# Performance work log

Measured on AMD Instinct MI355X. Metric: run time of the kernel, lower is better.

Reference implementation:

```python
import jax, jax.numpy as jnp
import numpy as np

N_HEAD = 8
N_VIEWS = 26
C = 256
H = W = 32
B_SCENE = 2


def _get_default_angles():
    # Reconstructed: bottom pole, top pole, then 3 rings of 8 azimuths at elev 45/0/-45.
    angs = [(0.0, -90.0), (0.0, 90.0)]
    for phi in (45.0, 0.0, -45.0):
        for k in range(8):
            angs.append((45.0 * k, phi))
    return np.array(angs)


def _angle_select():
    a = _get_default_angles()
    d = np.abs(a.reshape(26, 1, 2) - a.reshape(1, 26, 2))
    d = np.sum(np.minimum(d, 360 - d), axis=2)
    ab = d == 45
    ab[0, -8::2] = True
    ab[-8::2, 0] = True
    ab[1, 2:10:2] = True
    ab[2:10:2, 1] = True
    return [np.argwhere(ab[i]).reshape(-1) for i in range(26)]


def _mha_index(i):
    return i if i < 2 else (i - 2) // 8 + 2


def _mha(q, kv, Wqkv, bqkv, Wo, bo):
    # torch nn.MultiheadAttention, batch_first: packed in_proj, scale = 1/sqrt(head_dim)
    c = q.shape[-1]
    D = c // N_HEAD
    Wq, Wk, Wv = Wqkv[:c], Wqkv[c:2 * c], Wqkv[2 * c:]
    bq, bk, bv = bqkv[:c], bqkv[c:2 * c], bqkv[2 * c:]
    qp = q @ Wq.T + bq
    kp = kv @ Wk.T + bk
    vp = kv @ Wv.T + bv
    B, S, _ = qp.shape
    K = kp.shape[1]
    qh = qp.reshape(B, S, N_HEAD, D).transpose(0, 2, 1, 3)
    kh = kp.reshape(B, K, N_HEAD, D).transpose(0, 2, 1, 3)
    vh = vp.reshape(B, K, N_HEAD, D).transpose(0, 2, 1, 3)
    scores = jnp.einsum('bhqd,bhkd->bhqk', qh, kh) / jnp.sqrt(jnp.asarray(D, qh.dtype))
    att = jax.nn.softmax(scores, axis=-1)
    o = jnp.einsum('bhqk,bhkd->bhqd', att, vh).transpose(0, 2, 1, 3).reshape(B, S, c)
    return o @ Wo.T + bo


def setup_inputs() -> dict:
    key = jax.random.key(0)
    k1, k2, k3 = jax.random.split(key, 3)
    scale = 1.0 / np.sqrt(C)
    return {
        'x': jax.random.normal(k1, (B_SCENE * N_VIEWS, C, H, W), dtype=jnp.float32),
        'w_qkv': jax.random.normal(k2, (5, 3 * C, C), dtype=jnp.float32) * scale,
        'b_qkv': jnp.zeros((5, 3 * C), dtype=jnp.float32),
        'w_out': jax.random.normal(k3, (5, C, C), dtype=jnp.float32) * scale,
        'b_out': jnp.zeros((5, C), dtype=jnp.float32),
    }


def reference(x, w_qkv, b_qkv, w_out, b_out):
    bt, c, h, w = x.shape
    B = bt // N_VIEWS
    # (b t) c h w -> b t (h w) c
    xr = x.reshape(B, N_VIEWS, c, h * w).transpose(0, 1, 3, 2)
    sel = _angle_select()
    outs = []
    for i in range(N_VIEWS):
        m = _mha_index(i)
        q = xr[:, i]                                  # [B, S, c]
        kv = xr[:, sel[i]].reshape(B, -1, c)          # [B, n_nbr*S, c]
        outs.append(_mha(q, kv, w_qkv[m], b_qkv[m], w_out[m], b_out[m]))
    y = jnp.stack(outs, axis=1)                       # b t s c
    return y.transpose(0, 1, 3, 2).reshape(bt, c, h, w)
```

## Files before the change

kernel.cpp:

```cpp
#include <hip/hip_runtime.h>
#include <hip/hip_bf16.h>

#define NV 26
#define NS 1024
#define NC 256
#define NH 8
#define ND 32
#define NPAIR 66
#define PS 72

typedef unsigned short u16;
typedef unsigned int u32;
typedef short short8_t __attribute__((ext_vector_type(8)));
typedef float f32x4 __attribute__((ext_vector_type(4)));

__constant__ int c_view_m[NV]  = {0,1,2,2,2,2,2,2,2,2,3,3,3,3,3,3,3,3,4,4,4,4,4,4,4,4};
__constant__ int c_view_nk[NV] = {4,4,4,3,4,3,4,3,4,3,4,4,4,4,4,4,4,4,4,3,4,3,4,3,4,3};
__constant__ int c_view_kv[NV][4] = {
  {0,1,2,3},      {4,5,6,7},      {8,10,16,17},   {9,11,18,-1},
  {8,10,12,19},   {11,13,20,-1},  {8,12,14,21},   {13,15,22,-1},
  {8,14,16,23},   {9,15,24,-1},   {25,34,40,41},  {26,33,35,42},
  {27,34,36,43},  {28,35,37,44},  {29,36,38,45},  {30,37,39,46},
  {31,38,40,47},  {32,33,39,48},  {49,50,59,65},  {51,58,60,-1},
  {49,52,59,61},  {53,60,62,-1},  {49,54,61,63},  {55,62,64,-1},
  {49,56,63,65},  {57,58,64,-1}
};
__constant__ int c_pair_m[NPAIR] = {
  0,0,0,0, 1,1,1,1,
  2,2,2,2,2,2,2,2,2,2,2,2,2,2,2,2,2,
  3,3,3,3,3,3,3,3,3,3,3,3,3,3,3,3,3,3,3,3,3,3,3,3,
  4,4,4,4,4,4,4,4,4,4,4,4,4,4,4,4,4
};
__constant__ int c_pair_j[NPAIR] = {
  18,20,22,24, 2,4,6,8,
  1,2,3,4,5,6,7,8,9,10,11,12,13,14,15,16,17,
  2,3,4,5,6,7,8,9,10,11,12,13,14,15,16,17,18,19,20,21,22,23,24,25,
  0,10,11,12,13,14,15,16,17,18,19,20,21,22,23,24,25
};

__device__ __forceinline__ float bf16_to_f32(u16 u) {
  return __uint_as_float(((u32)u) << 16);
}
__device__ __forceinline__ u16 f32_to_bf16(float f) {
  u32 u = __float_as_uint(f);
  u32 r = (u + 0x7fffu + ((u >> 16) & 1u)) >> 16;
  return (u16)r;
}
__device__ __forceinline__ float ld_src(const void* p, size_t i, bool isf) {
  return isf ? ((const float*)p)[i] : bf16_to_f32(((const u16*)p)[i]);
}
__device__ __forceinline__ u32 pack_bf16x2_rne(float a, float b) {
  __hip_bfloat162 h = __float22bfloat162_rn(float2{a, b});
  return *(u32*)&h;
}
__device__ __forceinline__ bool detect_isf(const u16* __restrict__ x) {
  float f = fabsf(bf16_to_f32(x[threadIdx.x & 63]));
  if (!(f < 3.0e38f)) f = 3.0e38f;
#pragma unroll
  for (int m = 1; m < 64; m <<= 1) f = fmaxf(f, __shfl_xor(f, m));
  return f > 1.0e6f;
}

#define NW1 983040
#define NW2 327680
#define NB1 3840
#define NB2 1280
__global__ __launch_bounds__(256) void prep_w_kernel(const u16* __restrict__ xdet,
                                                     const void* __restrict__ w_qkv,
                                                     const void* __restrict__ w_out,
                                                     const void* __restrict__ b_qkv,
                                                     const void* __restrict__ b_out,
                                                     u16* __restrict__ Wqkvb, u16* __restrict__ Wob,
                                                     float* __restrict__ bq, float* __restrict__ bo) {
  bool isf = detect_isf(xdet);
  int i = blockIdx.x * 256 + threadIdx.x;
  if (i < NW1) Wqkvb[i] = f32_to_bf16(ld_src(w_qkv, i, isf));
  else if (i < NW1 + NW2) Wob[i - NW1] = f32_to_bf16(ld_src(w_out, i - NW1, isf));
  else if (i < NW1 + NW2 + NB1) bq[i - NW1 - NW2] = ld_src(b_qkv, i - NW1 - NW2, isf);
  else if (i < NW1 + NW2 + NB1 + NB2) bo[i - NW1 - NW2 - NB1] = ld_src(b_out, i - NW1 - NW2 - NB1, isf);
}

__global__ __launch_bounds__(256) void prep_x_kernel(const void* __restrict__ xin,
                                                     u16* __restrict__ Xt) {
  __shared__ float tile[32][33];
  bool isf = detect_isf((const u16*)xin);
  int bt = blockIdx.x;
  int s0 = blockIdx.y * 32, c0 = blockIdx.z * 32;
  int tid = threadIdx.x;
#pragma unroll
  for (int p = 0; p < 4; ++p) {
    int cl = (tid >> 5) + p * 8, sl = tid & 31;
    tile[cl][sl] = ld_src(xin, (size_t)(bt * NC + c0 + cl) * NS + s0 + sl, isf);
  }
  __syncthreads();
  int srow = tid >> 3, c4 = (tid & 7) * 4;
  ushort4 v;
  v.x = f32_to_bf16(tile[c4 + 0][srow]);
  v.y = f32_to_bf16(tile[c4 + 1][srow]);
  v.z = f32_to_bf16(tile[c4 + 2][srow]);
  v.w = f32_to_bf16(tile[c4 + 3][srow]);
  *(ushort4*)&Xt[(size_t)(bt * NS + s0 + srow) * NC + c0 + c4] = v;
}

__device__ __forceinline__ void gemm128(const u16* __restrict__ A, const u16* __restrict__ B,
                                        u16* As, u16* Bs, f32x4 acc[4][4],
                                        int wo, int ws, int lm, int g, int tid) {
#pragma unroll
  for (int i = 0; i < 4; ++i)
#pragma unroll
    for (int j = 0; j < 4; ++j)
#pragma unroll
      for (int r = 0; r < 4; ++r) acc[i][j][r] = 0.f;
  int c0i = tid, c1i = tid + 256;
  const u16* a0p = A + (c0i >> 2) * NC + (c0i & 3) * 8;
  const u16* a1p = A + (c1i >> 2) * NC + (c1i & 3) * 8;
  const u16* b0p = B + (c0i >> 2) * NC + (c0i & 3) * 8;
  const u16* b1p = B + (c1i >> 2) * NC + (c1i & 3) * 8;
  uint4 ra0 = *(const uint4*)(a0p);
  uint4 ra1 = *(const uint4*)(a1p);
  uint4 rb0 = *(const uint4*)(b0p);
  uint4 rb1 = *(const uint4*)(b1p);
  const u16* arow = As + (wo * 64 + lm) * 32 + g * 8;
  const u16* brow = Bs + (ws * 64 + lm) * 32 + g * 8;
#pragma unroll
  for (int k0 = 0; k0 < NC; k0 += 32) {
    __syncthreads();
    *(uint4*)&As[c0i * 8] = ra0;
    *(uint4*)&As[c1i * 8] = ra1;
    *(uint4*)&Bs[c0i * 8] = rb0;
    *(uint4*)&Bs[c1i * 8] = rb1;
    if (k0 + 32 < NC) {
      ra0 = *(const uint4*)(a0p + k0 + 32);
      ra1 = *(const uint4*)(a1p + k0 + 32);
      rb0 = *(const uint4*)(b0p + k0 + 32);
      rb1 = *(const uint4*)(b1p + k0 + 32);
    }
    __syncthreads();
    short8_t af[4], bf[4];
#pragma unroll
    for (int i = 0; i < 4; ++i) af[i] = *(const short8_t*)(arow + i * 16 * 32);
#pragma unroll
    for (int j = 0; j < 4; ++j) bf[j] = *(const short8_t*)(brow + j * 16 * 32);
#pragma unroll
    for (int i = 0; i < 4; ++i)
#pragma unroll
      for (int j = 0; j < 4; ++j)
        acc[i][j] = __builtin_amdgcn_mfma_f32_16x16x32_bf16(af[i], bf[j], acc[i][j], 0, 0, 0);
  }
}

__global__ __launch_bounds__(256, 3) void qkvproj_kernel(const u16* __restrict__ Xt,
                                                         const u16* __restrict__ Wqkvb,
                                                         const float* __restrict__ bq,
                                                         u16* __restrict__ Qb,
                                                         u16* __restrict__ Kb,
                                                         u16* __restrict__ Vb) {
  __shared__ __align__(16) u16 As[128 * 32];
  __shared__ __align__(16) u16 Bs[128 * 32];
  int bid = blockIdx.x;
  int tid = threadIdx.x;
  int wave = tid >> 6, lane = tid & 63, lm = lane & 15, g = lane >> 4;
  int wo = wave >> 1, ws = wave & 1;

  int obase, s0, m, src_bt;
  u16* dst; int dslot; float sc; bool isV = false;
  if (bid < 832) {
    int bt = bid >> 4, rem = bid & 15;
    obase = (rem & 1) * 128; s0 = (rem >> 1) * 128;
    m = c_view_m[bt % NV]; src_bt = bt;
    dst = Qb; dslot = bt; sc = 0.25505653862161186f;
  } else {
    int jb = bid - 832;
    int pb = jb >> 5, rem = jb & 31;
    int ot = rem & 3; s0 = (rem >> 2) * 128;
    obase = 256 + ot * 128;
    m = c_pair_m[pb >> 1]; src_bt = (pb & 1) * NV + c_pair_j[pb >> 1];
    dst = (ot < 2) ? Kb : Vb; dslot = pb; sc = 1.0f;
    isV = (ot >= 2);
  }
  f32x4 acc[4][4];
  gemm128(Wqkvb + (size_t)(m * 768 + obase) * NC,
          Xt + ((size_t)src_bt * NS + s0) * NC, As, Bs, acc, wo, ws, lm, g, tid);
  int osub = (obase < 256) ? 0 : ((obase < 512) ? 256 : 512);
#pragma unroll
  for (int i = 0; i < 4; ++i) {
    int o_r0 = obase + wo * 64 + i * 16 + 4 * g;
    float4 bias = *(const float4*)&bq[m * 768 + o_r0];
    int oloc = o_r0 - osub;
    int h = oloc >> 5, d0 = oloc & 31;
#pragma unroll
    for (int j = 0; j < 4; ++j) {
      int s = s0 + ws * 64 + j * 16 + lm;
      f32x4 c = acc[i][j];
      ushort4 v;
      v.x = f32_to_bf16((c[0] + bias.x) * sc);
      v.y = f32_to_bf16((c[1] + bias.y) * sc);
      v.z = f32_to_bf16((c[2] + bias.z) * sc);
      v.w = f32_to_bf16((c[3] + bias.w) * sc);
      if (isV) {
        u16* vt = dst + ((size_t)(dslot * NH + h) * ND + d0) * NS + s;
        vt[0]      = v.x;
        vt[NS]     = v.y;
        vt[2 * NS] = v.z;
        vt[3 * NS] = v.w;
      } else {
        *(ushort4*)&dst[((size_t)(dslot * NH + h) * NS + s) * ND + d0] = v;
      }
    }
  }
}

__global__ __launch_bounds__(256, 4) void attn_kernel(const u16* __restrict__ Qb,
                                                      const u16* __restrict__ Kb,
                                                      const u16* __restrict__ Vb,
                                                      u16* __restrict__ Ot) {
  int bt = blockIdx.x;
  int view = bt % NV;
  int b = bt / NV;
  int h = blockIdx.y;
  int tid = threadIdx.x;
  int wave = tid >> 6, lane = tid & 63;
  int lm = lane & 15, g = lane >> 4;
  int sbase = blockIdx.z * 256 + wave * 64;
  int nk = c_view_nk[view];

  __shared__ __align__(16) u16 Psm[4 * 2 * 16 * PS];

  short8_t qf[4];
  {
    const u16* qrow = Qb + ((size_t)(bt * NH + h) * NS + sbase) * ND;
#pragma unroll
    for (int qt = 0; qt < 4; ++qt)
      qf[qt] = *(const short8_t*)(qrow + (qt * 16 + lm) * ND + g * 8);
  }
  f32x4 accq[4][2];
  float l_acc[4] = {0.f, 0.f, 0.f, 0.f};
#pragma unroll
  for (int qt = 0; qt < 4; ++qt)
#pragma unroll
    for (int nt = 0; nt < 2; ++nt)
#pragma unroll
      for (int r = 0; r < 4; ++r) accq[qt][nt][r] = 0.f;

  u16* pwbase = Psm + wave * (2 * 16 * PS);
  int tot = nk * 16;

  for (int cc = 0; cc < tot; ++cc) {
    int nn = cc >> 4;
    int c0 = (cc & 15) * 64;
    int kvp = c_view_kv[view][nn];
    size_t off = (size_t)((kvp * 2 + b) * NH + h) * NS * ND;
    const u16* kp = Kb + off + (size_t)c0 * ND;
    const u16* vp = Vb + off + c0;

    short8_t kf[4];
#pragma unroll
    for (int kt = 0; kt < 4; ++kt)
      kf[kt] = *(const short8_t*)(kp + (kt * 16 + lm) * ND + g * 8);
    short8_t vfr[2][2];
#pragma unroll
    for (int nt = 0; nt < 2; ++nt)
#pragma unroll
      for (int k2 = 0; k2 < 2; ++k2)
        vfr[nt][k2] = *(const short8_t*)(vp + (size_t)(nt * 16 + lm) * NS + k2 * 32 + g * 8);

    __builtin_amdgcn_s_setprio(1);
#pragma unroll
    for (int qt = 0; qt < 4; ++qt) {
      u16* pw = pwbase + (qt & 1) * (16 * PS);
      f32x4 z4 = {0.f, 0.f, 0.f, 0.f};
      float ls = 0.f;
#pragma unroll
      for (int kt = 0; kt < 4; ++kt) {
        f32x4 s = __builtin_amdgcn_mfma_f32_16x16x32_bf16(kf[kt], qf[qt], z4, 0, 0, 0);
        float p0 = __builtin_amdgcn_exp2f(s[0]);
        float p1 = __builtin_amdgcn_exp2f(s[1]);
        float p2 = __builtin_amdgcn_exp2f(s[2]);
        float p3 = __builtin_amdgcn_exp2f(s[3]);
        ls += (p0 + p1) + (p2 + p3);
        uint2 w;
        w.x = pack_bf16x2_rne(p0, p1);
        w.y = pack_bf16x2_rne(p2, p3);
        *(uint2*)&pw[lm * PS + kt * 16 + g * 4] = w;
      }
      l_acc[qt] += ls;
      short8_t pf0 = *(const short8_t*)&pw[lm * PS + g * 8];
      short8_t pf1 = *(const short8_t*)&pw[lm * PS + 32 + g * 8];
      accq[qt][0] = __builtin_amdgcn_mfma_f32_16x16x32_bf16(pf0, vfr[0][0], accq[qt][0], 0, 0, 0);
      accq[qt][0] = __builtin_amdgcn_mfma_f32_16x16x32_bf16(pf1, vfr[0][1], accq[qt][0], 0, 0, 0);
      accq[qt][1] = __builtin_amdgcn_mfma_f32_16x16x32_bf16(pf0, vfr[1][0], accq[qt][1], 0, 0, 0);
      accq[qt][1] = __builtin_amdgcn_mfma_f32_16x16x32_bf16(pf1, vfr[1][1], accq[qt][1], 0, 0, 0);
    }
    __builtin_amdgcn_s_setprio(0);
  }

#pragma unroll
  for (int qt = 0; qt < 4; ++qt) {
    float l = l_acc[qt];
    l += __shfl_xor(l, 16);
    l += __shfl_xor(l, 32);
#pragma unroll
    for (int r = 0; r < 4; ++r) {
      float lr = __shfl(l, 20 * g + r);
      float inv = __builtin_amdgcn_rcpf(lr);
      int s = sbase + qt * 16 + 4 * g + r;
      u16* op = Ot + (size_t)(bt * NS + s) * NC + h * 32 + lm;
      op[0]  = f32_to_bf16(accq[qt][0][r] * inv);
      op[16] = f32_to_bf16(accq[qt][1][r] * inv);
    }
  }
}

__global__ __launch_bounds__(256, 3) void oproj_kernel(const u16* __restrict__ xdet,
                                                       const u16* __restrict__ Ot,
                                                       const u16* __restrict__ Wob,
                                                       const float* __restrict__ bo,
                                                       void* __restrict__ out) {
  __shared__ __align__(16) u16 As[128 * 32];
  __shared__ __align__(16) u16 Bs[128 * 32];
  bool isf = detect_isf(xdet);
  int bid = blockIdx.x;
  int bt = bid >> 4, rem = bid & 15;
  int obase = (rem & 1) * 128, s0 = (rem >> 1) * 128;
  int m = c_view_m[bt % NV];
  int tid = threadIdx.x;
  int wave = tid >> 6, lane = tid & 63, lm = lane & 15, g = lane >> 4;
  int wo = wave >> 1, ws = wave & 1;
  f32x4 acc[4][4];
  gemm128(Wob + (size_t)(m * NC + obase) * NC,
          Ot + ((size_t)bt * NS + s0) * NC, As, Bs, acc, wo, ws, lm, g, tid);
#pragma unroll
  for (int i = 0; i < 4; ++i) {
    int o_r0 = obase + wo * 64 + i * 16 + 4 * g;
    float4 bias = *(const float4*)&bo[m * NC + o_r0];
#pragma unroll
    for (int j = 0; j < 4; ++j) {
      int s = s0 + ws * 64 + j * 16 + lm;
      f32x4 c = acc[i][j];
      size_t base = (size_t)(bt * NC + o_r0) * NS + s;
      float v0 = c[0] + bias.x, v1 = c[1] + bias.y, v2 = c[2] + bias.z, v3 = c[3] + bias.w;
      if (isf) {
        float* fo = (float*)out;
        fo[base] = v0; fo[base + NS] = v1; fo[base + 2 * NS] = v2; fo[base + 3 * NS] = v3;
      } else {
        u16* ho = (u16*)out;
        ho[base] = f32_to_bf16(v0); ho[base + NS] = f32_to_bf16(v1);
        ho[base + 2 * NS] = f32_to_bf16(v2); ho[base + 3 * NS] = f32_to_bf16(v3);
      }
    }
  }
}


extern "C" void kernel_launch(void* const* d_in, const int* in_sizes, int n_in,
                              void* d_out, int out_size, void* d_ws, size_t ws_size,
                              hipStream_t stream) {
  (void)in_sizes; (void)n_in; (void)out_size;
  const void* x     = d_in[0];
  const void* w_qkv = d_in[1];
  const void* b_qkv = d_in[2];
  const void* w_out = d_in[3];
  const void* b_out = d_in[4];

  if (ws_size < 222842880ull) return;

  char* wsb = (char*)d_ws;
  float* bq    = (float*)(wsb + 0);
  float* bo    = (float*)(wsb + 15360);
  u16*   Wqkvb = (u16*)(wsb + 20480);
  u16*   Wob   = (u16*)(wsb + 1986560);
  u16*   Xt    = (u16*)(wsb + 2641920);
  u16*   Qb    = (u16*)(wsb + 29904896);
  u16*   Kb    = (u16*)(wsb + 57167872);
  u16*   Vb    = (u16*)(wsb + 126373888);
  u16*   Ot    = (u16*)(wsb + 195579904);

  prep_w_kernel<<<5140, 256, 0, stream>>>((const u16*)x, w_qkv, w_out, b_qkv, b_out,
                                          Wqkvb, Wob, bq, bo);
  prep_x_kernel<<<dim3(52, 32, 8), 256, 0, stream>>>(x, Xt);
  qkvproj_kernel<<<5056, 256, 0, stream>>>(Xt, Wqkvb, bq, Qb, Kb, Vb);
  attn_kernel<<<dim3(52, 8, 4), 256, 0, stream>>>(Qb, Kb, Vb, Ot);
  oproj_kernel<<<832, 256, 0, stream>>>((const u16*)x, Ot, Wob, bo, d_out);
}
```

Baseline: 573.2 us.

## Replace LDS round-trip of P with permlane swaps and MFMA row-sum

The attention kernel no longer writes the exponentiated score tile to shared memory and reads it back in A-operand layout. It rearranges the packed bf16 P values across lanes with v_permlane32_swap/v_permlane16_swap instead. The softmax denominator is now accumulated with two extra MFMAs against a ones vector rather than scalar adds plus final shuffles. This removes LDS traffic and waits, at the cost of extra MFMA work and more registers, so launch bounds drop from 4 to 3 blocks per CU. Because the row sums now come from the bf16-rounded P values, the normalisation changes slightly.

```diff
diff --git a/kernel.cpp b/kernel.cpp
--- a/kernel.cpp
+++ b/kernel.cpp
@@ -7,12 +7,12 @@
 #define NH 8
 #define ND 32
 #define NPAIR 66
-#define PS 72
 
 typedef unsigned short u16;
 typedef unsigned int u32;
 typedef short short8_t __attribute__((ext_vector_type(8)));
 typedef float f32x4 __attribute__((ext_vector_type(4)));
+typedef unsigned int u32x4 __attribute__((ext_vector_type(4)));
 
 __constant__ int c_view_m[NV]  = {0,1,2,2,2,2,2,2,2,2,3,3,3,3,3,3,3,3,4,4,4,4,4,4,4,4};
 __constant__ int c_view_nk[NV] = {4,4,4,3,4,3,4,3,4,3,4,4,4,4,4,4,4,4,4,3,4,3,4,3,4,3};
@@ -210,7 +210,7 @@
   }
 }
 
-__global__ __launch_bounds__(256, 4) void attn_kernel(const u16* __restrict__ Qb,
+__global__ __launch_bounds__(256, 3) void attn_kernel(const u16* __restrict__ Qb,
                                                       const u16* __restrict__ Kb,
                                                       const u16* __restrict__ Vb,
                                                       u16* __restrict__ Ot) {
@@ -224,8 +224,6 @@
   int sbase = blockIdx.z * 256 + wave * 64;
   int nk = c_view_nk[view];
 
-  __shared__ __align__(16) u16 Psm[4 * 2 * 16 * PS];
-
   short8_t qf[4];
   {
     const u16* qrow = Qb + ((size_t)(bt * NH + h) * NS + sbase) * ND;
@@ -234,15 +232,16 @@
       qf[qt] = *(const short8_t*)(qrow + (qt * 16 + lm) * ND + g * 8);
   }
   f32x4 accq[4][2];
-  float l_acc[4] = {0.f, 0.f, 0.f, 0.f};
-#pragma unroll
-  for (int qt = 0; qt < 4; ++qt)
-#pragma unroll
-    for (int nt = 0; nt < 2; ++nt)
-#pragma unroll
-      for (int r = 0; r < 4; ++r) accq[qt][nt][r] = 0.f;
-
-  u16* pwbase = Psm + wave * (2 * 16 * PS);
+  f32x4 acc_l[4];
+#pragma unroll
+  for (int qt = 0; qt < 4; ++qt) {
+#pragma unroll
+    for (int r = 0; r < 4; ++r) { accq[qt][0][r] = 0.f; accq[qt][1][r] = 0.f; acc_l[qt][r] = 0.f; }
+  }
+  short8_t ones;
+#pragma unroll
+  for (int e = 0; e < 8; ++e) ones[e] = (short)0x3F80;
+
   int tot = nk * 16;
 
   for (int cc = 0; cc < tot; ++cc) {
@@ -267,42 +266,52 @@
     __builtin_amdgcn_s_setprio(1);
 #pragma unroll
     for (int qt = 0; qt < 4; ++qt) {
-      u16* pw = pwbase + (qt & 1) * (16 * PS);
       f32x4 z4 = {0.f, 0.f, 0.f, 0.f};
-      float ls = 0.f;
+      f32x4 sv[4];
+#pragma unroll
+      for (int kt = 0; kt < 4; ++kt)
+        sv[kt] = __builtin_amdgcn_mfma_f32_16x16x32_bf16(kf[kt], qf[qt], z4, 0, 0, 0);
+      u32 w[4][2];
 #pragma unroll
       for (int kt = 0; kt < 4; ++kt) {
-        f32x4 s = __builtin_amdgcn_mfma_f32_16x16x32_bf16(kf[kt], qf[qt], z4, 0, 0, 0);
-        float p0 = __builtin_amdgcn_exp2f(s[0]);
-        float p1 = __builtin_amdgcn_exp2f(s[1]);
-        float p2 = __builtin_amdgcn_exp2f(s[2]);
-        float p3 = __builtin_amdgcn_exp2f(s[3]);
-        ls += (p0 + p1) + (p2 + p3);
-        uint2 w;
-        w.x = pack_bf16x2_rne(p0, p1);
-        w.y = pack_bf16x2_rne(p2, p3);
-        *(uint2*)&pw[lm * PS + kt * 16 + g * 4] = w;
+        float p0 = __builtin_amdgcn_exp2f(sv[kt][0]);
+        float p1 = __builtin_amdgcn_exp2f(sv[kt][1]);
+        float p2 = __builtin_amdgcn_exp2f(sv[kt][2]);
+        float p3 = __builtin_amdgcn_exp2f(sv[kt][3]);
+        w[kt][0] = pack_bf16x2_rne(p0, p1);
+        w[kt][1] = pack_bf16x2_rne(p2, p3);
       }
-      l_acc[qt] += ls;
-      short8_t pf0 = *(const short8_t*)&pw[lm * PS + g * 8];
-      short8_t pf1 = *(const short8_t*)&pw[lm * PS + 32 + g * 8];
+      u32 pa[2][4];
+#pragma unroll
+      for (int kt1 = 0; kt1 < 2; ++kt1) {
+#pragma unroll
+        for (int hh = 0; hh < 2; ++hh) {
+          u32 X = w[2 * kt1][hh], Y = w[2 * kt1 + 1][hh];
+          asm("v_permlane32_swap_b32 %0, %1" : "+v"(X), "+v"(Y));
+          asm("v_permlane16_swap_b32 %0, %1" : "+v"(X), "+v"(Y));
+          pa[kt1][hh] = X;
+          pa[kt1][2 + hh] = Y;
+        }
+      }
+      u32x4 a0 = {pa[0][0], pa[0][1], pa[0][2], pa[0][3]};
+      u32x4 a1 = {pa[1][0], pa[1][1], pa[1][2], pa[1][3]};
+      short8_t pf0 = __builtin_bit_cast(short8_t, a0);
+      short8_t pf1 = __builtin_bit_cast(short8_t, a1);
       accq[qt][0] = __builtin_amdgcn_mfma_f32_16x16x32_bf16(pf0, vfr[0][0], accq[qt][0], 0, 0, 0);
       accq[qt][0] = __builtin_amdgcn_mfma_f32_16x16x32_bf16(pf1, vfr[0][1], accq[qt][0], 0, 0, 0);
       accq[qt][1] = __builtin_amdgcn_mfma_f32_16x16x32_bf16(pf0, vfr[1][0], accq[qt][1], 0, 0, 0);
       accq[qt][1] = __builtin_amdgcn_mfma_f32_16x16x32_bf16(pf1, vfr[1][1], accq[qt][1], 0, 0, 0);
+      acc_l[qt]   = __builtin_amdgcn_mfma_f32_16x16x32_bf16(pf0, ones, acc_l[qt], 0, 0, 0);
+      acc_l[qt]   = __builtin_amdgcn_mfma_f32_16x16x32_bf16(pf1, ones, acc_l[qt], 0, 0, 0);
     }
     __builtin_amdgcn_s_setprio(0);
   }
 
 #pragma unroll
   for (int qt = 0; qt < 4; ++qt) {
-    float l = l_acc[qt];
-    l += __shfl_xor(l, 16);
-    l += __shfl_xor(l, 32);
 #pragma unroll
     for (int r = 0; r < 4; ++r) {
-      float lr = __shfl(l, 20 * g + r);
-      float inv = __builtin_amdgcn_rcpf(lr);
+      float inv = __builtin_amdgcn_rcpf(acc_l[qt][r]);
       int s = sbase + qt * 16 + 4 * g + r;
       u16* op = Ot + (size_t)(bt * NS + s) * NC + h * 32 + lm;
       op[0]  = f32_to_bf16(accq[qt][0][r] * inv);
```

New measurement: 621.8 us. 1.08x slower.
